# Performance work log

Hardware: AMD Instinct MI355X
Metric: run time of the kernel (lower is better)

## Reference

```python
import jax, jax.numpy as jnp
import numpy as np

B, C_IN, C_OUT = 32, 64, 128
K_SIZE, STRIDE, PAD, H = 3, 1, 1, 56
H_OUT = (H + 2 * PAD - K_SIZE) // STRIDE + 1


def setup_inputs() -> dict:
    key = jax.random.key(0)
    kx, kw = jax.random.split(key)
    x = jax.random.normal(kx, (B, C_IN, H, H), dtype=jnp.float32)
    # kaiming_uniform-ish init for K of shape [kh, kw, C_in, C_out]
    fan_in = K_SIZE * C_IN * C_OUT  # torch fan_in for this layout (dim1 * receptive field)
    bound = np.sqrt(6.0 / fan_in).astype(np.float32)
    K = jax.random.uniform(kw, (K_SIZE, K_SIZE, C_IN, C_OUT), dtype=jnp.float32,
                           minval=-bound, maxval=bound)
    return {"x": x, "K": K}


def reference(x, K):
    # Faithful to the torch code INCLUDING its mismatched flatten orders:
    #   patch flattened as (C_in, kh, kw); K flattened as (kh, kw, C_in).
    xp = jnp.pad(x, ((0, 0), (0, 0), (PAD, PAD), (PAD, PAD)))
    end = (H_OUT - 1) * STRIDE + 1
    # patches[b, c, di, dj, i, j] = xp[b, c, i*stride+di, j*stride+dj]
    rows = []
    for di in range(K_SIZE):
        cols = []
        for dj in range(K_SIZE):
            cols.append(xp[:, :, di:di + end:STRIDE, dj:dj + end:STRIDE])  # [B,C,Ho,Wo]
        rows.append(jnp.stack(cols, axis=2))  # [B,C,kw,Ho,Wo]
    patches = jnp.stack(rows, axis=2)  # [B, C, kh, kw, Ho, Wo]
    # flatten patch in (C, kh, kw) order -> [B, Ho, Wo, C*kh*kw]
    p = patches.transpose(0, 4, 5, 1, 2, 3).reshape(B, H_OUT, H_OUT, -1)
    # K flattened in (kh, kw, C) order, exactly as K.view(-1, out_channels)
    Kf = K.reshape(-1, C_OUT)  # [kh*kw*C_in, C_out]
    out = p @ Kf  # [B, Ho, Wo, C_out]
    return out.transpose(0, 3, 1, 2)  # [B, C_out, Ho, Wo]
```

## Files before the change

kernel.cpp:

```cpp
#include <hip/hip_runtime.h>
#include <hip/hip_bf16.h>
#include <stdint.h>


#define B_   32
#define CIN  64
#define COUT 128
#define H_   56
#define HP   58
#define F_   576

typedef __attribute__((ext_vector_type(8))) short bf16x8;
typedef __attribute__((ext_vector_type(4))) float f32x4;

#define XP_ELEMS (B_*HP*HP*CIN)
#define XP_SLACK 4096
#define XP_TOTAL (XP_ELEMS + XP_SLACK)
#define WG_ELEMS (COUT*F_)
#define WS_NEEDED ((size_t)(XP_TOTAL + WG_ELEMS) * 2)

__global__ __launch_bounds__(256) void prep_x(const float* __restrict__ x,
                                              __hip_bfloat16* __restrict__ xpT) {
  const int id = blockIdx.x;
  const int t  = threadIdx.x;
  if (id >= B_*HP) {
    for (int idx = t; idx < XP_SLACK; idx += 256)
      xpT[XP_ELEMS + idx] = __float2bfloat16(0.f);
    return;
  }
  const int b = id / HP, h = id % HP;
  __hip_bfloat16* orow = xpT + (size_t)(b*HP + h) * HP * CIN;
  if (h == 0 || h == HP-1) {
    for (int idx = t; idx < HP*CIN; idx += 256) orow[idx] = __float2bfloat16(0.f);
    return;
  }
  __shared__ float tile[CIN][H_ + 1];
  const float* xrow = x + ((size_t)(b*CIN)*H_ + (h-1)) * H_;
  for (int idx = t; idx < CIN*H_; idx += 256) {
    int c = idx / H_, w = idx % H_;
    tile[c][w] = xrow[(size_t)c*H_*H_ + w];
  }
  __syncthreads();
  for (int idx = t; idx < HP*CIN; idx += 256) {
    int w = idx >> 6, c = idx & 63;
    float v = (w == 0 || w == HP-1) ? 0.f : tile[c][w-1];
    orow[idx] = __float2bfloat16(v);
  }
}

__global__ __launch_bounds__(256) void prep_w(const float* __restrict__ K,
                                              __hip_bfloat16* __restrict__ WgT) {
  int n = blockIdx.x*256 + threadIdx.x;
  if (n >= WG_ELEMS) return;
  int co = n / F_, g = n % F_;
  int di = g / 192, dj = (g % 192) / 64, c = g & 63;
  int f  = c*9 + di*3 + dj;
  int kh = f / 192, kw = (f % 192) / 64, cc = f & 63;
  float v = K[(((size_t)kh*3 + kw)*CIN + cc)*COUT + co];
  WgT[n] = __float2bfloat16(v);
}

__global__ __launch_bounds__(256, 2) void conv_mfma(
    const __hip_bfloat16* __restrict__ xpT,
    const __hip_bfloat16* __restrict__ WgT,
    float* __restrict__ out) {
  __shared__ __align__(16) char lds[49152];
  const int t    = threadIdx.x;
  const int wave = t >> 6;
  const int l    = t & 63;
  const int lr   = l & 15, lq = l >> 4;
  const int wr   = wave >> 1, wc = wave & 1;
  const int bb   = blockIdx.x / H_;
  const int i    = blockIdx.x % H_;

  f32x4 acc[2][4];
#pragma unroll
  for (int mi = 0; mi < 2; ++mi)
#pragma unroll
    for (int ni = 0; ni < 4; ++ni) acc[mi][ni] = (f32x4)0.f;

  const char* wbase = (const char*)WgT;

  auto stage = [&](int q, int buf) {
    const int di = q / 3, dj = q % 3;
    const char* ag = (const char*)(xpT + ((size_t)(bb*HP + (i + di))*HP + dj) * CIN);
    char* Ab = lds + buf*8192;
    char* Bb = lds + 16384 + buf*16384;
#pragma unroll
    for (int s = 0; s < 2; ++s) {
      int o = s*4096 + t*16;
      int m = o >> 7;
      int src = (o & ~127) | ((o & 127) ^ ((m & 7) << 4));
      __builtin_amdgcn_global_load_lds(
          (const __attribute__((address_space(1))) void*)(ag + src),
          (__attribute__((address_space(3))) void*)(Ab + s*4096 + wave*1024),
          16, 0, 0);
    }
    const char* wg = wbase + q*128;
#pragma unroll
    for (int s = 0; s < 4; ++s) {
      int o = s*4096 + t*16;
      int co = o >> 7;
      int scb = (o & 127) ^ ((co & 7) << 4);
      __builtin_amdgcn_global_load_lds(
          (const __attribute__((address_space(1))) void*)(wg + (size_t)co*1152 + scb),
          (__attribute__((address_space(3))) void*)(Bb + s*4096 + wave*1024),
          16, 0, 0);
    }
  };

  stage(0, 0);
  __syncthreads();

  for (int q = 0; q < 9; ++q) {
    const int buf = q & 1;
    if (q + 1 < 9) stage(q + 1, buf ^ 1);
    const char* Ab = lds + buf*8192;
    const char* Bb = lds + 16384 + buf*16384;
#pragma unroll
    for (int ks = 0; ks < 2; ++ks) {
      bf16x8 a[2], bfr[4];
      const int cb = ks*64 + lq*16;
#pragma unroll
      for (int mi = 0; mi < 2; ++mi) {
        int m = wr*32 + mi*16 + lr;
        int addr = ((m << 7) | cb) ^ ((m & 7) << 4);
        a[mi] = *(const bf16x8*)(Ab + addr);
      }
#pragma unroll
      for (int ni = 0; ni < 4; ++ni) {
        int co = wc*64 + ni*16 + lr;
        int addr = ((co << 7) | cb) ^ ((co & 7) << 4);
        bfr[ni] = *(const bf16x8*)(Bb + addr);
      }
#pragma unroll
      for (int mi = 0; mi < 2; ++mi)
#pragma unroll
        for (int ni = 0; ni < 4; ++ni)
          acc[mi][ni] = __builtin_amdgcn_mfma_f32_16x16x32_bf16(
              a[mi], bfr[ni], acc[mi][ni], 0, 0, 0);
    }
    __syncthreads();
  }

#pragma unroll
  for (int mi = 0; mi < 2; ++mi) {
    int j0 = wr*32 + mi*16 + lq*4;
    if (j0 < H_) {
#pragma unroll
      for (int ni = 0; ni < 4; ++ni) {
        int co = wc*64 + ni*16 + lr;
        float* dst = out + (((size_t)(bb*COUT + co))*H_ + i)*H_ + j0;
        *(f32x4*)dst = acc[mi][ni];
      }
    }
  }
}

__global__ __launch_bounds__(256) void conv_naive(const float* __restrict__ x,
                                                  const float* __restrict__ K,
                                                  float* __restrict__ out) {
  int idx = blockIdx.x*256 + threadIdx.x;
  const int total = B_*COUT*H_*H_;
  if (idx >= total) return;
  int j = idx % H_, i = (idx / H_) % H_, co = (idx / (H_*H_)) % COUT, b = idx / (H_*H_*COUT);
  float s = 0.f;
  for (int c = 0; c < CIN; ++c)
    for (int di = 0; di < 3; ++di) {
      int ii = i + di - 1;
      if (ii < 0 || ii >= H_) continue;
      for (int dj = 0; dj < 3; ++dj) {
        int jj = j + dj - 1;
        if (jj < 0 || jj >= H_) continue;
        int f = c*9 + di*3 + dj;
        int kh = f / 192, kw = (f % 192) / 64, cc = f & 63;
        s += x[(((size_t)b*CIN + c)*H_ + ii)*H_ + jj] *
             K[(((size_t)kh*3 + kw)*CIN + cc)*COUT + co];
      }
    }
  out[idx] = s;
}

extern "C" void kernel_launch(void* const* d_in, const int* in_sizes, int n_in,
                              void* d_out, int out_size, void* d_ws, size_t ws_size,
                              hipStream_t stream) {
  const float* x = (const float*)d_in[0];
  const float* K = (const float*)d_in[1];
  float* out = (float*)d_out;
  if (ws_size >= WS_NEEDED) {
    __hip_bfloat16* xpT = (__hip_bfloat16*)d_ws;
    __hip_bfloat16* WgT = xpT + XP_TOTAL;
    prep_x<<<B_*HP + 1, 256, 0, stream>>>(x, xpT);
    prep_w<<<(WG_ELEMS + 255)/256, 256, 0, stream>>>(K, WgT);
    conv_mfma<<<B_*H_, 256, 0, stream>>>(xpT, WgT, out);
  } else {
    conv_naive<<<(B_*COUT*H_*H_ + 255)/256, 256, 0, stream>>>(x, K, out);
  }
}
```

Baseline: 45.99 us.

## Merge prep kernels, vectorize prep, and double conv tile to two output rows

```diff
diff --git a/kernel.cpp b/kernel.cpp
--- a/kernel.cpp
+++ b/kernel.cpp
@@ -19,91 +19,110 @@
 #define WG_ELEMS (COUT*F_)
 #define WS_NEEDED ((size_t)(XP_TOTAL + WG_ELEMS) * 2)
 
-__global__ __launch_bounds__(256) void prep_x(const float* __restrict__ x,
-                                              __hip_bfloat16* __restrict__ xpT) {
+#define NROW   (B_*HP)
+#define NWBLK  (WG_ELEMS/256)
+
+__global__ __launch_bounds__(256) void prep_all(const float* __restrict__ x,
+                                                const float* __restrict__ K,
+                                                __hip_bfloat16* __restrict__ xpT,
+                                                __hip_bfloat16* __restrict__ WgT) {
   const int id = blockIdx.x;
   const int t  = threadIdx.x;
-  if (id >= B_*HP) {
-    for (int idx = t; idx < XP_SLACK; idx += 256)
-      xpT[XP_ELEMS + idx] = __float2bfloat16(0.f);
+
+  if (id > NROW) {
+    int n = (id - (NROW + 1))*256 + t;
+    int co = n / F_, g = n % F_;
+    int di = g / 192, dj = (g % 192) / 64, c = g & 63;
+    int f  = c*9 + di*3 + dj;
+    int kh = f / 192, kw = (f % 192) / 64, cc = f & 63;
+    WgT[n] = __float2bfloat16(K[(((size_t)kh*3 + kw)*CIN + cc)*COUT + co]);
     return;
   }
+  if (id == NROW) {
+    bf16x8 z = (bf16x8)0;
+    for (int idx = t; idx < XP_SLACK/8; idx += 256)
+      ((bf16x8*)(xpT + XP_ELEMS))[idx] = z;
+    return;
+  }
+
   const int b = id / HP, h = id % HP;
   __hip_bfloat16* orow = xpT + (size_t)(b*HP + h) * HP * CIN;
   if (h == 0 || h == HP-1) {
-    for (int idx = t; idx < HP*CIN; idx += 256) orow[idx] = __float2bfloat16(0.f);
+    bf16x8 z = (bf16x8)0;
+    for (int idx = t; idx < HP*CIN/8; idx += 256) ((bf16x8*)orow)[idx] = z;
     return;
   }
-  __shared__ float tile[CIN][H_ + 1];
+  __shared__ __align__(16) float tile[CIN][60];
   const float* xrow = x + ((size_t)(b*CIN)*H_ + (h-1)) * H_;
-  for (int idx = t; idx < CIN*H_; idx += 256) {
-    int c = idx / H_, w = idx % H_;
-    tile[c][w] = xrow[(size_t)c*H_*H_ + w];
+  for (int idx = t; idx < CIN*(H_/4); idx += 256) {
+    int c = idx / 14, w4 = idx % 14;
+    f32x4 v = *(const f32x4*)(xrow + (size_t)c*H_*H_ + w4*4);
+    *(f32x4*)&tile[c][w4*4] = v;
   }
   __syncthreads();
-  for (int idx = t; idx < HP*CIN; idx += 256) {
-    int w = idx >> 6, c = idx & 63;
-    float v = (w == 0 || w == HP-1) ? 0.f : tile[c][w-1];
-    orow[idx] = __float2bfloat16(v);
-  }
-}
-
-__global__ __launch_bounds__(256) void prep_w(const float* __restrict__ K,
-                                              __hip_bfloat16* __restrict__ WgT) {
-  int n = blockIdx.x*256 + threadIdx.x;
-  if (n >= WG_ELEMS) return;
-  int co = n / F_, g = n % F_;
-  int di = g / 192, dj = (g % 192) / 64, c = g & 63;
-  int f  = c*9 + di*3 + dj;
-  int kh = f / 192, kw = (f % 192) / 64, cc = f & 63;
-  float v = K[(((size_t)kh*3 + kw)*CIN + cc)*COUT + co];
-  WgT[n] = __float2bfloat16(v);
+  for (int idx = t; idx < HP*8; idx += 256) {
+    int w = idx >> 3, cg = (idx & 7) * 8;
+    __align__(16) __hip_bfloat16 tmp[8];
+    if (w == 0 || w == HP-1) {
+#pragma unroll
+      for (int k2 = 0; k2 < 8; ++k2) tmp[k2] = __float2bfloat16(0.f);
+    } else {
+#pragma unroll
+      for (int k2 = 0; k2 < 8; ++k2) tmp[k2] = __float2bfloat16(tile[cg + k2][w-1]);
+    }
+    *(bf16x8*)(orow + (size_t)w*CIN + cg) = *(const bf16x8*)tmp;
+  }
 }
 
 __global__ __launch_bounds__(256, 2) void conv_mfma(
     const __hip_bfloat16* __restrict__ xpT,
     const __hip_bfloat16* __restrict__ WgT,
     float* __restrict__ out) {
-  __shared__ __align__(16) char lds[49152];
+  __shared__ __align__(16) char lds[65536];
   const int t    = threadIdx.x;
   const int wave = t >> 6;
   const int l    = t & 63;
   const int lr   = l & 15, lq = l >> 4;
   const int wr   = wave >> 1, wc = wave & 1;
-  const int bb   = blockIdx.x / H_;
-  const int i    = blockIdx.x % H_;
-
-  f32x4 acc[2][4];
-#pragma unroll
-  for (int mi = 0; mi < 2; ++mi)
+
+  const int bid = blockIdx.x;
+  const int swz = (bid & 7) * 112 + (bid >> 3);
+  const int bb  = swz / 28;
+  const int i0  = (swz % 28) * 2;
+
+  f32x4 acc[4][4];
+#pragma unroll
+  for (int mi = 0; mi < 4; ++mi)
 #pragma unroll
     for (int ni = 0; ni < 4; ++ni) acc[mi][ni] = (f32x4)0.f;
 
+  const char* xb    = (const char*)xpT + (size_t)bb*HP*HP*CIN*2;
   const char* wbase = (const char*)WgT;
 
   auto stage = [&](int q, int buf) {
     const int di = q / 3, dj = q % 3;
-    const char* ag = (const char*)(xpT + ((size_t)(bb*HP + (i + di))*HP + dj) * CIN);
-    char* Ab = lds + buf*8192;
-    char* Bb = lds + 16384 + buf*16384;
-#pragma unroll
-    for (int s = 0; s < 2; ++s) {
+    char* Ab = lds + buf*32768;
+    char* Bb = Ab + 16384;
+#pragma unroll
+    for (int s = 0; s < 4; ++s) {
       int o = s*4096 + t*16;
       int m = o >> 7;
-      int src = (o & ~127) | ((o & 127) ^ ((m & 7) << 4));
+      const char* src = xb
+          + (size_t)((i0 + (m >> 6) + di)*HP + dj + (m & 63)) * (CIN*2)
+          + ((o & 127) ^ ((m & 7) << 4));
       __builtin_amdgcn_global_load_lds(
-          (const __attribute__((address_space(1))) void*)(ag + src),
+          (const __attribute__((address_space(1))) void*)src,
           (__attribute__((address_space(3))) void*)(Ab + s*4096 + wave*1024),
           16, 0, 0);
     }
     const char* wg = wbase + q*128;
 #pragma unroll
     for (int s = 0; s < 4; ++s) {
-      int o = s*4096 + t*16;
+      int o  = s*4096 + t*16;
       int co = o >> 7;
-      int scb = (o & 127) ^ ((co & 7) << 4);
+      const char* src = wg + (size_t)co*1152 + ((o & 127) ^ ((co & 7) << 4));
       __builtin_amdgcn_global_load_lds(
-          (const __attribute__((address_space(1))) void*)(wg + (size_t)co*1152 + scb),
+          (const __attribute__((address_space(1))) void*)src,
           (__attribute__((address_space(3))) void*)(Bb + s*4096 + wave*1024),
           16, 0, 0);
     }
@@ -115,26 +134,24 @@
   for (int q = 0; q < 9; ++q) {
     const int buf = q & 1;
     if (q + 1 < 9) stage(q + 1, buf ^ 1);
-    const char* Ab = lds + buf*8192;
-    const char* Bb = lds + 16384 + buf*16384;
+    const char* Ab = lds + buf*32768;
+    const char* Bb = Ab + 16384;
 #pragma unroll
     for (int ks = 0; ks < 2; ++ks) {
-      bf16x8 a[2], bfr[4];
+      bf16x8 a[4], bfr[4];
       const int cb = ks*64 + lq*16;
 #pragma unroll
-      for (int mi = 0; mi < 2; ++mi) {
-        int m = wr*32 + mi*16 + lr;
-        int addr = ((m << 7) | cb) ^ ((m & 7) << 4);
-        a[mi] = *(const bf16x8*)(Ab + addr);
+      for (int mi = 0; mi < 4; ++mi) {
+        int m = wr*64 + mi*16 + lr;
+        a[mi] = *(const bf16x8*)(Ab + (((m << 7) | cb) ^ ((m & 7) << 4)));
       }
 #pragma unroll
       for (int ni = 0; ni < 4; ++ni) {
         int co = wc*64 + ni*16 + lr;
-        int addr = ((co << 7) | cb) ^ ((co & 7) << 4);
-        bfr[ni] = *(const bf16x8*)(Bb + addr);
-      }
-#pragma unroll
-      for (int mi = 0; mi < 2; ++mi)
+        bfr[ni] = *(const bf16x8*)(Bb + (((co << 7) | cb) ^ ((co & 7) << 4)));
+      }
+#pragma unroll
+      for (int mi = 0; mi < 4; ++mi)
 #pragma unroll
         for (int ni = 0; ni < 4; ++ni)
           acc[mi][ni] = __builtin_amdgcn_mfma_f32_16x16x32_bf16(
@@ -144,9 +161,10 @@
   }
 
 #pragma unroll
-  for (int mi = 0; mi < 2; ++mi) {
-    int j0 = wr*32 + mi*16 + lq*4;
+  for (int mi = 0; mi < 4; ++mi) {
+    int j0 = mi*16 + lq*4;
     if (j0 < H_) {
+      int i = i0 + wr;
 #pragma unroll
       for (int ni = 0; ni < 4; ++ni) {
         int co = wc*64 + ni*16 + lr;
@@ -190,9 +208,8 @@
   if (ws_size >= WS_NEEDED) {
     __hip_bfloat16* xpT = (__hip_bfloat16*)d_ws;
     __hip_bfloat16* WgT = xpT + XP_TOTAL;
-    prep_x<<<B_*HP + 1, 256, 0, stream>>>(x, xpT);
-    prep_w<<<(WG_ELEMS + 255)/256, 256, 0, stream>>>(K, WgT);
-    conv_mfma<<<B_*H_, 256, 0, stream>>>(xpT, WgT, out);
+    prep_all<<<NROW + 1 + NWBLK, 256, 0, stream>>>(x, K, xpT, WgT);
+    conv_mfma<<<B_*28, 256, 0, stream>>>(xpT, WgT, out);
   } else {
     conv_naive<<<(B_*COUT*H_*H_ + 255)/256, 256, 0, stream>>>(x, K, out);
   }
```

Result: faster. 42.86 us (-6.8%).
